# Performance work log

Measured on AMD Instinct MI355X. Metric: run time of the kernel, lower is better.

The kernel has to match this reference:

```python
import math
import jax, jax.numpy as jnp
import numpy as np

IMAGE_SIZE = 224


def _resize_bilinear(img, out_h, out_w):
    """PyTorch F.interpolate(mode='bilinear', align_corners=False) equivalent.
    img: [B, H, W] -> [B, out_h, out_w]. No antialiasing (matches torch default)."""
    B, H, W = img.shape

    def coords(out, size):
        r = jnp.maximum((jnp.arange(out, dtype=jnp.float32) + 0.5) * (size / out) - 0.5, 0.0)
        i0 = jnp.minimum(jnp.floor(r).astype(jnp.int32), size - 1)
        i1 = jnp.minimum(i0 + 1, size - 1)
        w = r - i0.astype(jnp.float32)
        return i0, i1, w

    r0, r1, wr = coords(out_h, H)
    c0, c1, wc = coords(out_w, W)
    rows = img[:, r0, :] * (1.0 - wr)[None, :, None] + img[:, r1, :] * wr[None, :, None]
    out = rows[:, :, c0] * (1.0 - wc)[None, None, :] + rows[:, :, c1] * wc[None, None, :]
    return out


def _normalize_minmax(x, eps=1e-8):
    mn = x.min()
    mx = x.max()
    return jnp.where(mx - mn < eps, jnp.zeros_like(x), (x - mn) / (mx - mn + eps))


def _grid_embed(vals, n):
    """Row-major scatter of vals[:, :n] into a ceil(sqrt(n))^2 grid (zero padded)."""
    B = vals.shape[0]
    gs = int(math.ceil(math.sqrt(n)))
    pad = gs * gs - n
    return jnp.pad(vals, ((0, 0), (0, pad))).reshape(B, gs, gs)


def setup_inputs() -> dict:
    key = jax.random.key(0)
    hidden_state = jax.random.normal(key, (32, 512, 4096, 1), dtype=jnp.float32)
    return {"hidden_state": hidden_state}


def reference(hidden_state):
    B, E, N, _ = hidden_state.shape
    x = hidden_state[..., 0]  # [B, E, N]

    # temporal view: mean over nodes -> [B, E] -> grid -> resize
    t_grid = _grid_embed(x.mean(axis=2), E)
    temporal = _normalize_minmax(_resize_bilinear(t_grid, IMAGE_SIZE, IMAGE_SIZE))

    # spatial view: mean over embedding dim -> [B, N] -> grid -> resize
    s_grid = _grid_embed(x.mean(axis=1), N)
    spatial = _normalize_minmax(_resize_bilinear(s_grid, IMAGE_SIZE, IMAGE_SIZE))

    # correlation view: row-normalized centered features, [B, E, E] correlation
    xc = x - x.mean(axis=2, keepdims=True)
    xn = xc / (jnp.linalg.norm(xc, axis=2, keepdims=True) + 1e-8)
    corr = jnp.einsum('bin,bjn->bij', xn, xn)  # [B, E, E]
    correlation = _normalize_minmax(_resize_bilinear(corr, IMAGE_SIZE, IMAGE_SIZE))

    # [B, 3, image_size, image_size]
    return jnp.stack([temporal, spatial, correlation], axis=1)
```

## Files before the change

### kernel.cpp

```cpp
#include <hip/hip_runtime.h>
#include <hip/hip_bf16.h>
#include <math.h>

#define IMG 224
#define PIX (IMG*IMG)
#define B_ 32
#define E_ 512
#define N_ 4096
#define SV_BLOCKS 256
#define SC_ ((float)(512.0/224.0))
#define RPB 16
#define NCHUNK 32
#define KSPLIT 2
#define KLEN (N_/KSPLIT)
#define NTILE 10

typedef __attribute__((ext_vector_type(8))) short bf16x8;
typedef __attribute__((ext_vector_type(4))) float f32x4;

__device__ inline unsigned short f2bf(float f){
  unsigned u = __float_as_uint(f);
  unsigned r = (u + 0x7FFFu + ((u >> 16) & 1u)) >> 16;
  return (unsigned short)r;
}

__global__ void __launch_bounds__(256) stats_y(const float* __restrict__ x,
                                               float* __restrict__ meanv,
                                               float* __restrict__ colpart,
                                               ushort* __restrict__ y){
  int b = blockIdx.x >> 5, chunk = blockIdx.x & 31;
  int e0 = chunk << 4;
  int t = threadIdx.x;
  __shared__ short sInv[512];
  __shared__ float sW[224];
  __shared__ float red[2][16];
  sInv[t] = -1; sInv[t + 256] = -1;
  __syncthreads();
  if (t < 224){
    float r = fmaxf(((float)t + 0.5f) * SC_ - 0.5f, 0.f);
    int r0 = min((int)r, E_ - 1);
    sW[t] = r - (float)r0;
    sInv[r0] = (short)t;
  }
  __syncthreads();

  float cur[16], prev[16], nxt[16], csum[16];
  #pragma unroll
  for (int j = 0; j < 16; j++){ csum[j] = 0.f; prev[j] = 0.f; }
  const float4* row0 = (const float4*)(x + ((size_t)b * E_ + e0) * N_);
  #pragma unroll
  for (int k = 0; k < 4; k++) *(float4*)(cur + 4 * k) = row0[t + 256 * k];
  float pmu = 0.f, prn = 0.f;

  for (int idx = 0; idx <= RPB; idx++){
    int e = e0 + idx;
    if (e >= E_) break;
    bool hasNext = (idx < RPB) && (e + 1 < E_);
    if (hasNext){
      const float4* nr = (const float4*)(x + ((size_t)b * E_ + e + 1) * N_);
      #pragma unroll
      for (int k = 0; k < 4; k++) *(float4*)(nxt + 4 * k) = nr[t + 256 * k];
    }
    float s = 0.f, ss = 0.f;
    #pragma unroll
    for (int j = 0; j < 16; j++){ s += cur[j]; ss += cur[j] * cur[j]; }
    #pragma unroll
    for (int o = 32; o; o >>= 1){ s += __shfl_down(s, o); ss += __shfl_down(ss, o); }
    int wv = t >> 6, ln = t & 63, p = idx & 1;
    if (ln == 0){ red[p][wv] = s; red[p][8 + wv] = ss; }
    __syncthreads();
    float S  = red[p][0] + red[p][1] + red[p][2] + red[p][3];
    float SS = red[p][8] + red[p][9] + red[p][10] + red[p][11];
    float mu = S * (1.f / N_);
    float var = fmaxf(SS - S * S * (1.f / N_), 0.f);
    float rn = 1.f / (sqrtf(var) + 1e-8f);
    if (idx < RPB){
      #pragma unroll
      for (int j = 0; j < 16; j++) csum[j] += cur[j];
      if (t == 0) meanv[b * E_ + e] = mu;
    }
    if (idx >= 1){
      int i = sInv[e - 1];
      if (i >= 0){
        float w = sW[i];
        float a0 = (1.f - w) * prn, a1 = w * rn;
        float cc = -(a0 * pmu + a1 * mu);
        ushort* yo = y + ((size_t)b * IMG + i) * N_;
        #pragma unroll
        for (int k = 0; k < 4; k++){
          union { ushort u[4]; int2 v; } pk;
          #pragma unroll
          for (int j = 0; j < 4; j++)
            pk.u[j] = f2bf(a0 * prev[4*k+j] + a1 * cur[4*k+j] + cc);
          *(int2*)(yo + 1024 * k + 4 * t) = pk.v;
        }
      }
    }
    pmu = mu; prn = rn;
    #pragma unroll
    for (int j = 0; j < 16; j++){ prev[j] = cur[j]; if (hasNext) cur[j] = nxt[j]; }
  }
  float* cp = colpart + ((size_t)(b * NCHUNK + chunk)) * N_;
  #pragma unroll
  for (int k = 0; k < 4; k++) *(float4*)(cp + 1024 * k + 4 * t) = *(float4*)(csum + 4 * k);
}

__global__ void __launch_bounds__(256) col_finalize(const float* __restrict__ colpart,
                                                    float* __restrict__ colmean){
  int b = blockIdx.x >> 4;
  int n = ((blockIdx.x & 15) << 8) + threadIdx.x;
  float s = 0.f;
  #pragma unroll
  for (int c = 0; c < NCHUNK; c++) s += colpart[((size_t)(b * NCHUNK + c)) * N_ + n];
  colmean[b * N_ + n] = s * (1.f / E_);
}

__device__ inline float grid_val(const float* v, int gs, int n, int r, int c){
  int idx = r * gs + c;
  return (idx < n) ? v[idx] : 0.f;
}
__device__ inline float bilin(const float* v, int gs, int n, int i, int j){
  float sc = (float)((double)gs / 224.0);
  float r = fmaxf(((float)i + 0.5f) * sc - 0.5f, 0.f);
  float c = fmaxf(((float)j + 0.5f) * sc - 0.5f, 0.f);
  int r0 = min((int)r, gs - 1), c0 = min((int)c, gs - 1);
  int r1 = min(r0 + 1, gs - 1), c1 = min(c0 + 1, gs - 1);
  float wr = r - (float)r0, wc = c - (float)c0;
  float v00 = grid_val(v, gs, n, r0, c0), v10 = grid_val(v, gs, n, r1, c0);
  float v01 = grid_val(v, gs, n, r0, c1), v11 = grid_val(v, gs, n, r1, c1);
  float ra = v00 * (1.f - wr) + v10 * wr;
  float rb = v01 * (1.f - wr) + v11 * wr;
  return ra * (1.f - wc) + rb * wc;
}

__global__ void __launch_bounds__(256) sv_minmax(const float* __restrict__ meanv,
                                                 const float* __restrict__ colmean,
                                                 float* __restrict__ scr){
  float tmn = INFINITY, tmx = -INFINITY, smn = INFINITY, smx = -INFINITY;
  for (int g = blockIdx.x * 256 + threadIdx.x; g < B_ * PIX; g += SV_BLOCKS * 256){
    int b = g / PIX, p = g - b * PIX;
    int i = p / IMG, j = p - i * IMG;
    float tv = bilin(meanv   + b * E_, 23, E_, i, j);
    float sv = bilin(colmean + b * N_, 64, N_, i, j);
    tmn = fminf(tmn, tv); tmx = fmaxf(tmx, tv);
    smn = fminf(smn, sv); smx = fmaxf(smx, sv);
  }
  #pragma unroll
  for (int o = 32; o; o >>= 1){
    tmn = fminf(tmn, __shfl_down(tmn, o)); tmx = fmaxf(tmx, __shfl_down(tmx, o));
    smn = fminf(smn, __shfl_down(smn, o)); smx = fmaxf(smx, __shfl_down(smx, o));
  }
  __shared__ float red[4][4];
  int wv = threadIdx.x >> 6, ln = threadIdx.x & 63;
  if (ln == 0){ red[wv][0] = tmn; red[wv][1] = tmx; red[wv][2] = smn; red[wv][3] = smx; }
  __syncthreads();
  if (threadIdx.x == 0){
    scr[blockIdx.x * 4 + 0] = fminf(fminf(red[0][0], red[1][0]), fminf(red[2][0], red[3][0]));
    scr[blockIdx.x * 4 + 1] = fmaxf(fmaxf(red[0][1], red[1][1]), fmaxf(red[2][1], red[3][1]));
    scr[blockIdx.x * 4 + 2] = fminf(fminf(red[0][2], red[1][2]), fminf(red[2][2], red[3][2]));
    scr[blockIdx.x * 4 + 3] = fmaxf(fmaxf(red[0][3], red[1][3]), fmaxf(red[2][3], red[3][3]));
  }
}

#define LDSTR 72
__device__ const int TI_[NTILE] = {0,0,0,0,1,1,1,2,2,3};
__device__ const int TJ_[NTILE] = {0,1,2,3,1,2,3,2,3,3};

__global__ void __launch_bounds__(256) corr_gemm_sk(const ushort* __restrict__ y,
                                                    float* __restrict__ partials){
  int bt = blockIdx.x % (B_ * NTILE);
  int ks = blockIdx.x / (B_ * NTILE);
  int b = bt / NTILE, tile = bt - b * NTILE;
  int ti = TI_[tile], tj = TJ_[tile];
  const ushort* yb = y + (size_t)b * IMG * N_ + (size_t)ks * KLEN;
  __shared__ ushort lA[64 * LDSTR];
  __shared__ ushort lB[64 * LDSTR];
  int t = threadIdx.x;
  int wv = t >> 6, ln = t & 63;
  int wm = wv & 1, wn = wv >> 1;
  int quad = ln >> 4, l16 = ln & 15;
  f32x4 acc[2][2] = {};
  int s = t & 7, r2 = t >> 3;
  int rA0 = min(ti * 64 + r2,      223), rA1 = min(ti * 64 + r2 + 32, 223);
  int rB0 = min(tj * 64 + r2,      223), rB1 = min(tj * 64 + r2 + 32, 223);
  for (int k0 = 0; k0 < KLEN; k0 += 64){
    int4 a0 = *(const int4*)(yb + (size_t)rA0 * N_ + k0 + s * 8);
    int4 a1 = *(const int4*)(yb + (size_t)rA1 * N_ + k0 + s * 8);
    int4 b0v = *(const int4*)(yb + (size_t)rB0 * N_ + k0 + s * 8);
    int4 b1v = *(const int4*)(yb + (size_t)rB1 * N_ + k0 + s * 8);
    __syncthreads();
    *(int4*)(lA + r2 * LDSTR + s * 8)        = a0;
    *(int4*)(lA + (r2 + 32) * LDSTR + s * 8) = a1;
    *(int4*)(lB + r2 * LDSTR + s * 8)        = b0v;
    *(int4*)(lB + (r2 + 32) * LDSTR + s * 8) = b1v;
    __syncthreads();
    #pragma unroll
    for (int kk = 0; kk < 2; kk++){
      bf16x8 af0 = *(const bf16x8*)(lA + (wm * 32 + l16)      * LDSTR + kk * 32 + quad * 8);
      bf16x8 af1 = *(const bf16x8*)(lA + (wm * 32 + 16 + l16) * LDSTR + kk * 32 + quad * 8);
      bf16x8 bf0 = *(const bf16x8*)(lB + (wn * 32 + l16)      * LDSTR + kk * 32 + quad * 8);
      bf16x8 bf1 = *(const bf16x8*)(lB + (wn * 32 + 16 + l16) * LDSTR + kk * 32 + quad * 8);
      acc[0][0] = __builtin_amdgcn_mfma_f32_16x16x32_bf16(af0, bf0, acc[0][0], 0, 0, 0);
      acc[0][1] = __builtin_amdgcn_mfma_f32_16x16x32_bf16(af0, bf1, acc[0][1], 0, 0, 0);
      acc[1][0] = __builtin_amdgcn_mfma_f32_16x16x32_bf16(af1, bf0, acc[1][0], 0, 0, 0);
      acc[1][1] = __builtin_amdgcn_mfma_f32_16x16x32_bf16(af1, bf1, acc[1][1], 0, 0, 0);
    }
  }
  float* pp = partials + ((size_t)ks * (B_ * NTILE) + bt) * 4096 + t * 16;
  #pragma unroll
  for (int im = 0; im < 2; im++)
    #pragma unroll
    for (int in = 0; in < 2; in++)
      *(f32x4*)(pp + 4 * (im * 2 + in)) = acc[im][in];
}

__global__ void __launch_bounds__(256) corr_reduce(const float* __restrict__ partials,
                                                   float* __restrict__ out,
                                                   float* __restrict__ scr){
  int bt = blockIdx.x;
  int b = bt / NTILE, tile = bt - b * NTILE;
  int ti = TI_[tile], tj = TJ_[tile];
  bool diag = (ti == tj);
  int t = threadIdx.x;
  int wv = t >> 6, ln = t & 63;
  int wm = wv & 1, wn = wv >> 1;
  int quad = ln >> 4, l16 = ln & 15;
  f32x4 acc[2][2];
  #pragma unroll
  for (int im = 0; im < 2; im++)
    #pragma unroll
    for (int in = 0; in < 2; in++){
      f32x4 a = {0.f, 0.f, 0.f, 0.f};
      #pragma unroll
      for (int ks = 0; ks < KSPLIT; ks++)
        a += *(const f32x4*)(partials + ((size_t)ks * (B_ * NTILE) + bt) * 4096
                             + t * 16 + 4 * (im * 2 + in));
      acc[im][in] = a;
    }
  float mn = INFINITY, mx = -INFINITY;
  float* ov = out + ((size_t)b * 3 + 2) * PIX;
  #pragma unroll
  for (int im = 0; im < 2; im++)
    #pragma unroll
    for (int in = 0; in < 2; in++){
      int gi0 = ti * 64 + wm * 32 + im * 16 + quad * 4;
      int gj  = tj * 64 + wn * 32 + in * 16 + l16;
      #pragma unroll
      for (int rg = 0; rg < 4; rg++){
        int gi = gi0 + rg;
        if (gi < IMG && gj < IMG){
          float v = acc[im][in][rg];
          ov[gi * IMG + gj] = v;
          mn = fminf(mn, v); mx = fmaxf(mx, v);
        }
      }
      if (!diag && gj < IMG && gi0 < IMG){
        float4 tv;
        tv.x = acc[im][in][0]; tv.y = acc[im][in][1];
        tv.z = acc[im][in][2]; tv.w = acc[im][in][3];
        *(float4*)(ov + gj * IMG + gi0) = tv;
      }
    }
  #pragma unroll
  for (int o = 32; o; o >>= 1){
    mn = fminf(mn, __shfl_down(mn, o)); mx = fmaxf(mx, __shfl_down(mx, o));
  }
  __shared__ float red[4][2];
  if (ln == 0){ red[wv][0] = mn; red[wv][1] = mx; }
  __syncthreads();
  if (t == 0){
    scr[bt * 2 + 0] = fminf(fminf(red[0][0], red[1][0]), fminf(red[2][0], red[3][0]));
    scr[bt * 2 + 1] = fmaxf(fmaxf(red[0][1], red[1][1]), fmaxf(red[2][1], red[3][1]));
  }
}

__global__ void __launch_bounds__(256) reduce_slots(const float* __restrict__ sv_scr,
                                                    const float* __restrict__ corr_scr,
                                                    float* __restrict__ slots){
  int t = threadIdx.x;
  float tmn = sv_scr[4*t+0], tmx = sv_scr[4*t+1];
  float smn = sv_scr[4*t+2], smx = sv_scr[4*t+3];
  float cmn = INFINITY, cmx = -INFINITY;
  for (int idx = t; idx < B_ * NTILE; idx += 256){
    cmn = fminf(cmn, corr_scr[2*idx]);
    cmx = fmaxf(cmx, corr_scr[2*idx+1]);
  }
  #pragma unroll
  for (int o = 32; o; o >>= 1){
    tmn = fminf(tmn, __shfl_down(tmn, o)); tmx = fmaxf(tmx, __shfl_down(tmx, o));
    smn = fminf(smn, __shfl_down(smn, o)); smx = fmaxf(smx, __shfl_down(smx, o));
    cmn = fminf(cmn, __shfl_down(cmn, o)); cmx = fmaxf(cmx, __shfl_down(cmx, o));
  }
  __shared__ float red[4][6];
  int wv = t >> 6, ln = t & 63;
  if (ln == 0){
    red[wv][0]=tmn; red[wv][1]=tmx; red[wv][2]=smn;
    red[wv][3]=smx; red[wv][4]=cmn; red[wv][5]=cmx;
  }
  __syncthreads();
  if (t == 0){
    slots[0] = fminf(fminf(red[0][0],red[1][0]), fminf(red[2][0],red[3][0]));
    slots[1] = fmaxf(fmaxf(red[0][1],red[1][1]), fmaxf(red[2][1],red[3][1]));
    slots[2] = fminf(fminf(red[0][2],red[1][2]), fminf(red[2][2],red[3][2]));
    slots[3] = fmaxf(fmaxf(red[0][3],red[1][3]), fmaxf(red[2][3],red[3][3]));
    slots[4] = fminf(fminf(red[0][4],red[1][4]), fminf(red[2][4],red[3][4]));
    slots[5] = fmaxf(fmaxf(red[0][5],red[1][5]), fmaxf(red[2][5],red[3][5]));
  }
}

__global__ void __launch_bounds__(256) final_write(const float* __restrict__ meanv,
                                                   const float* __restrict__ colmean,
                                                   float* __restrict__ out,
                                                   const float* __restrict__ slots){
  int g = blockIdx.x * 256 + threadIdx.x;
  float tmn = slots[0], tmx = slots[1];
  float smn = slots[2], smx = slots[3];
  int b = g / PIX, p = g - b * PIX;
  int i = p / IMG, j = p - i * IMG;
  float tv = bilin(meanv   + b * E_, 23, E_, i, j);
  float sv = bilin(colmean + b * N_, 64, N_, i, j);
  float td = tmx - tmn, sd = smx - smn;
  out[((size_t)b * 3 + 0) * PIX + p] = (td < 1e-8f) ? 0.f : (tv - tmn) / (td + 1e-8f);
  out[((size_t)b * 3 + 1) * PIX + p] = (sd < 1e-8f) ? 0.f : (sv - smn) / (sd + 1e-8f);
  if (g < B_ * PIX / 4){
    float cmn = slots[4], cmx = slots[5];
    float cd = cmx - cmn;
    float inv = 1.f / (cd + 1e-8f);
    bool z = cd < 1e-8f;
    int c = g * 4;
    int bb = c / PIX, pp = c - bb * PIX;
    float* oc = out + ((size_t)bb * 3 + 2) * PIX + pp;
    float4 v = *(float4*)oc;
    v.x = z ? 0.f : (v.x - cmn) * inv;
    v.y = z ? 0.f : (v.y - cmn) * inv;
    v.z = z ? 0.f : (v.z - cmn) * inv;
    v.w = z ? 0.f : (v.w - cmn) * inv;
    *(float4*)oc = v;
  }
}

extern "C" void kernel_launch(void* const* d_in, const int* in_sizes, int n_in,
                              void* d_out, int out_size, void* d_ws, size_t ws_size,
                              hipStream_t stream){
  const float* x = (const float*)d_in[0];
  float* out = (float*)d_out;
  char* ws = (char*)d_ws;
  float* slots    = (float*)(ws + 0);
  float* meanv    = (float*)(ws + 256);
  float* colmean  = meanv + B_ * E_;
  float* colpart  = colmean + B_ * N_;
  float* sv_scr   = colpart + (size_t)B_ * NCHUNK * N_;
  float* corr_scr = sv_scr + SV_BLOCKS * 4;
  size_t y_off = ((size_t)((char*)(corr_scr + B_ * NTILE * 2) - ws) + 255) & ~(size_t)255;
  ushort* y = (ushort*)(ws + y_off);
  size_t p_off = (y_off + (size_t)B_ * IMG * N_ * 2 + 255) & ~(size_t)255;
  float* partials = (float*)(ws + p_off);

  hipLaunchKernelGGL(stats_y, dim3(B_ * NCHUNK), dim3(256), 0, stream,
                     x, meanv, colpart, y);
  hipLaunchKernelGGL(corr_gemm_sk, dim3(KSPLIT * B_ * NTILE), dim3(256), 0, stream,
                     y, partials);
  hipLaunchKernelGGL(corr_reduce, dim3(B_ * NTILE), dim3(256), 0, stream,
                     partials, out, corr_scr);
  hipLaunchKernelGGL(col_finalize, dim3(B_ * 16), dim3(256), 0, stream,
                     colpart, colmean);
  hipLaunchKernelGGL(sv_minmax, dim3(SV_BLOCKS), dim3(256), 0, stream,
                     meanv, colmean, sv_scr);
  hipLaunchKernelGGL(reduce_slots, dim3(1), dim3(256), 0, stream,
                     sv_scr, corr_scr, slots);
  hipLaunchKernelGGL(final_write, dim3(B_ * PIX / 256), dim3(256), 0, stream,
                     meanv, colmean, out, slots);
}
```

Measured before the change: 446.0 us.

## Fuse correlation GEMM and reduce with 128x128 tiles and double-buffered LDS

Replaces the split-K 64x64-tile correlation GEMM plus separate partial-reduce kernel with one kernel that computes full-K 128x128 upper-triangle tiles (3 per batch) and writes the output and min/max directly. Loads are register-prefetched and LDS is double-buffered, so only one barrier is needed per k-step. This drops the partials buffer round-trip and a launch, and raises MFMA reuse per LDS load. In exchange it launches only 96 blocks, which is far fewer than the number of CUs, uses more registers for the 4x4 accumulators, and does extra wasted work in the padded region beyond row 224.

```diff
diff --git a/kernel.cpp b/kernel.cpp
--- a/kernel.cpp
+++ b/kernel.cpp
@@ -11,9 +11,8 @@
 #define SC_ ((float)(512.0/224.0))
 #define RPB 16
 #define NCHUNK 32
-#define KSPLIT 2
-#define KLEN (N_/KSPLIT)
-#define NTILE 10
+#define NT2 3
+#define LDSTR2 72
 
 typedef __attribute__((ext_vector_type(8))) short bf16x8;
 typedef __attribute__((ext_vector_type(4))) float f32x4;
@@ -162,89 +161,75 @@
   }
 }
 
-#define LDSTR 72
-__device__ const int TI_[NTILE] = {0,0,0,0,1,1,1,2,2,3};
-__device__ const int TJ_[NTILE] = {0,1,2,3,1,2,3,2,3,3};
-
-__global__ void __launch_bounds__(256) corr_gemm_sk(const ushort* __restrict__ y,
-                                                    float* __restrict__ partials){
-  int bt = blockIdx.x % (B_ * NTILE);
-  int ks = blockIdx.x / (B_ * NTILE);
-  int b = bt / NTILE, tile = bt - b * NTILE;
-  int ti = TI_[tile], tj = TJ_[tile];
-  const ushort* yb = y + (size_t)b * IMG * N_ + (size_t)ks * KLEN;
-  __shared__ ushort lA[64 * LDSTR];
-  __shared__ ushort lB[64 * LDSTR];
+__device__ const int TI2_[NT2] = {0, 0, 1};
+__device__ const int TJ2_[NT2] = {0, 1, 1};
+
+__global__ void __launch_bounds__(256) corr_gemm_f(const ushort* __restrict__ y,
+                                                   float* __restrict__ out,
+                                                   float* __restrict__ scr){
+  int b = blockIdx.x / NT2, tile = blockIdx.x - b * NT2;
+  int ti = TI2_[tile], tj = TJ2_[tile];
+  bool diag = (ti == tj);
+  const ushort* yb = y + (size_t)b * IMG * N_;
+  __shared__ ushort lA[2][128 * LDSTR2];
+  __shared__ ushort lB[2][128 * LDSTR2];
   int t = threadIdx.x;
   int wv = t >> 6, ln = t & 63;
   int wm = wv & 1, wn = wv >> 1;
   int quad = ln >> 4, l16 = ln & 15;
-  f32x4 acc[2][2] = {};
-  int s = t & 7, r2 = t >> 3;
-  int rA0 = min(ti * 64 + r2,      223), rA1 = min(ti * 64 + r2 + 32, 223);
-  int rB0 = min(tj * 64 + r2,      223), rB1 = min(tj * 64 + r2 + 32, 223);
-  for (int k0 = 0; k0 < KLEN; k0 += 64){
-    int4 a0 = *(const int4*)(yb + (size_t)rA0 * N_ + k0 + s * 8);
-    int4 a1 = *(const int4*)(yb + (size_t)rA1 * N_ + k0 + s * 8);
-    int4 b0v = *(const int4*)(yb + (size_t)rB0 * N_ + k0 + s * 8);
-    int4 b1v = *(const int4*)(yb + (size_t)rB1 * N_ + k0 + s * 8);
+  int s8 = t & 7, r0 = t >> 3;
+  f32x4 acc[4][4] = {};
+  int rA[4], rB[4];
+  #pragma unroll
+  for (int q = 0; q < 4; q++){
+    rA[q] = min(ti * 128 + r0 + 32 * q, IMG - 1);
+    rB[q] = min(tj * 128 + r0 + 32 * q, IMG - 1);
+  }
+  int4 ra[4], rb[4];
+  #pragma unroll
+  for (int q = 0; q < 4; q++){
+    ra[q] = *(const int4*)(yb + (size_t)rA[q] * N_ + s8 * 8);
+    rb[q] = *(const int4*)(yb + (size_t)rB[q] * N_ + s8 * 8);
+  }
+  for (int s = 0; s < 64; s++){
+    int cur = s & 1;
+    #pragma unroll
+    for (int q = 0; q < 4; q++){
+      *(int4*)(lA[cur] + (r0 + 32 * q) * LDSTR2 + s8 * 8) = ra[q];
+      *(int4*)(lB[cur] + (r0 + 32 * q) * LDSTR2 + s8 * 8) = rb[q];
+    }
+    if (s + 1 < 64){
+      int k0 = (s + 1) * 64;
+      #pragma unroll
+      for (int q = 0; q < 4; q++){
+        ra[q] = *(const int4*)(yb + (size_t)rA[q] * N_ + k0 + s8 * 8);
+        rb[q] = *(const int4*)(yb + (size_t)rB[q] * N_ + k0 + s8 * 8);
+      }
+    }
     __syncthreads();
-    *(int4*)(lA + r2 * LDSTR + s * 8)        = a0;
-    *(int4*)(lA + (r2 + 32) * LDSTR + s * 8) = a1;
-    *(int4*)(lB + r2 * LDSTR + s * 8)        = b0v;
-    *(int4*)(lB + (r2 + 32) * LDSTR + s * 8) = b1v;
-    __syncthreads();
     #pragma unroll
     for (int kk = 0; kk < 2; kk++){
-      bf16x8 af0 = *(const bf16x8*)(lA + (wm * 32 + l16)      * LDSTR + kk * 32 + quad * 8);
-      bf16x8 af1 = *(const bf16x8*)(lA + (wm * 32 + 16 + l16) * LDSTR + kk * 32 + quad * 8);
-      bf16x8 bf0 = *(const bf16x8*)(lB + (wn * 32 + l16)      * LDSTR + kk * 32 + quad * 8);
-      bf16x8 bf1 = *(const bf16x8*)(lB + (wn * 32 + 16 + l16) * LDSTR + kk * 32 + quad * 8);
-      acc[0][0] = __builtin_amdgcn_mfma_f32_16x16x32_bf16(af0, bf0, acc[0][0], 0, 0, 0);
-      acc[0][1] = __builtin_amdgcn_mfma_f32_16x16x32_bf16(af0, bf1, acc[0][1], 0, 0, 0);
-      acc[1][0] = __builtin_amdgcn_mfma_f32_16x16x32_bf16(af1, bf0, acc[1][0], 0, 0, 0);
-      acc[1][1] = __builtin_amdgcn_mfma_f32_16x16x32_bf16(af1, bf1, acc[1][1], 0, 0, 0);
-    }
-  }
-  float* pp = partials + ((size_t)ks * (B_ * NTILE) + bt) * 4096 + t * 16;
-  #pragma unroll
-  for (int im = 0; im < 2; im++)
-    #pragma unroll
-    for (int in = 0; in < 2; in++)
-      *(f32x4*)(pp + 4 * (im * 2 + in)) = acc[im][in];
-}
-
-__global__ void __launch_bounds__(256) corr_reduce(const float* __restrict__ partials,
-                                                   float* __restrict__ out,
-                                                   float* __restrict__ scr){
-  int bt = blockIdx.x;
-  int b = bt / NTILE, tile = bt - b * NTILE;
-  int ti = TI_[tile], tj = TJ_[tile];
-  bool diag = (ti == tj);
-  int t = threadIdx.x;
-  int wv = t >> 6, ln = t & 63;
-  int wm = wv & 1, wn = wv >> 1;
-  int quad = ln >> 4, l16 = ln & 15;
-  f32x4 acc[2][2];
-  #pragma unroll
-  for (int im = 0; im < 2; im++)
-    #pragma unroll
-    for (int in = 0; in < 2; in++){
-      f32x4 a = {0.f, 0.f, 0.f, 0.f};
-      #pragma unroll
-      for (int ks = 0; ks < KSPLIT; ks++)
-        a += *(const f32x4*)(partials + ((size_t)ks * (B_ * NTILE) + bt) * 4096
-                             + t * 16 + 4 * (im * 2 + in));
-      acc[im][in] = a;
-    }
+      bf16x8 af[4], bf[4];
+      #pragma unroll
+      for (int m = 0; m < 4; m++){
+        af[m] = *(const bf16x8*)(lA[cur] + (wm * 64 + m * 16 + l16) * LDSTR2 + kk * 32 + quad * 8);
+        bf[m] = *(const bf16x8*)(lB[cur] + (wn * 64 + m * 16 + l16) * LDSTR2 + kk * 32 + quad * 8);
+      }
+      #pragma unroll
+      for (int im = 0; im < 4; im++)
+        #pragma unroll
+        for (int in = 0; in < 4; in++)
+          acc[im][in] = __builtin_amdgcn_mfma_f32_16x16x32_bf16(af[im], bf[in], acc[im][in], 0, 0, 0);
+    }
+  }
   float mn = INFINITY, mx = -INFINITY;
   float* ov = out + ((size_t)b * 3 + 2) * PIX;
   #pragma unroll
-  for (int im = 0; im < 2; im++)
-    #pragma unroll
-    for (int in = 0; in < 2; in++){
-      int gi0 = ti * 64 + wm * 32 + im * 16 + quad * 4;
-      int gj  = tj * 64 + wn * 32 + in * 16 + l16;
+  for (int im = 0; im < 4; im++){
+    #pragma unroll
+    for (int in = 0; in < 4; in++){
+      int gi0 = ti * 128 + wm * 64 + im * 16 + quad * 4;
+      int gj  = tj * 128 + wn * 64 + in * 16 + l16;
       #pragma unroll
       for (int rg = 0; rg < 4; rg++){
         int gi = gi0 + rg;
@@ -261,6 +246,7 @@
         *(float4*)(ov + gj * IMG + gi0) = tv;
       }
     }
+  }
   #pragma unroll
   for (int o = 32; o; o >>= 1){
     mn = fminf(mn, __shfl_down(mn, o)); mx = fmaxf(mx, __shfl_down(mx, o));
@@ -269,8 +255,8 @@
   if (ln == 0){ red[wv][0] = mn; red[wv][1] = mx; }
   __syncthreads();
   if (t == 0){
-    scr[bt * 2 + 0] = fminf(fminf(red[0][0], red[1][0]), fminf(red[2][0], red[3][0]));
-    scr[bt * 2 + 1] = fmaxf(fmaxf(red[0][1], red[1][1]), fmaxf(red[2][1], red[3][1]));
+    scr[blockIdx.x * 2 + 0] = fminf(fminf(red[0][0], red[1][0]), fminf(red[2][0], red[3][0]));
+    scr[blockIdx.x * 2 + 1] = fmaxf(fmaxf(red[0][1], red[1][1]), fmaxf(red[2][1], red[3][1]));
   }
 }
 
@@ -281,7 +267,7 @@
   float tmn = sv_scr[4*t+0], tmx = sv_scr[4*t+1];
   float smn = sv_scr[4*t+2], smx = sv_scr[4*t+3];
   float cmn = INFINITY, cmx = -INFINITY;
-  for (int idx = t; idx < B_ * NTILE; idx += 256){
+  for (int idx = t; idx < B_ * NT2; idx += 256){
     cmn = fminf(cmn, corr_scr[2*idx]);
     cmx = fmaxf(cmx, corr_scr[2*idx+1]);
   }
@@ -351,17 +337,13 @@
   float* colpart  = colmean + B_ * N_;
   float* sv_scr   = colpart + (size_t)B_ * NCHUNK * N_;
   float* corr_scr = sv_scr + SV_BLOCKS * 4;
-  size_t y_off = ((size_t)((char*)(corr_scr + B_ * NTILE * 2) - ws) + 255) & ~(size_t)255;
+  size_t y_off = ((size_t)((char*)(corr_scr + B_ * NT2 * 2) - ws) + 255) & ~(size_t)255;
   ushort* y = (ushort*)(ws + y_off);
-  size_t p_off = (y_off + (size_t)B_ * IMG * N_ * 2 + 255) & ~(size_t)255;
-  float* partials = (float*)(ws + p_off);
 
   hipLaunchKernelGGL(stats_y, dim3(B_ * NCHUNK), dim3(256), 0, stream,
                      x, meanv, colpart, y);
-  hipLaunchKernelGGL(corr_gemm_sk, dim3(KSPLIT * B_ * NTILE), dim3(256), 0, stream,
-                     y, partials);
-  hipLaunchKernelGGL(corr_reduce, dim3(B_ * NTILE), dim3(256), 0, stream,
-                     partials, out, corr_scr);
+  hipLaunchKernelGGL(corr_gemm_f, dim3(B_ * NT2), dim3(256), 0, stream,
+                     y, out, corr_scr);
   hipLaunchKernelGGL(col_finalize, dim3(B_ * 16), dim3(256), 0, stream,
                      colpart, colmean);
   hipLaunchKernelGGL(sv_minmax, dim3(SV_BLOCKS), dim3(256), 0, stream,
```

After: 560.4 us. 1.26x slower.
